# Optimization experiments

Measured on AMD Instinct MI355X. Metric: run time of the kernel, lower is better.

## Reference

```python
import jax, jax.numpy as jnp
import numpy as np
from functools import partial

BANK = 256
ADDR = 64
OUT_C, IN_C, KH, KW = 64, 64, 3, 3
BS, H, W = 32, 128, 128


def setup_inputs() -> dict:
    key = jax.random.key(0)
    ks = jax.random.split(key, 6)
    x = jax.random.normal(ks[0], (BS, IN_C, H, W), dtype=jnp.float32)
    w_addr = jax.random.normal(ks[1], (BS, ADDR), dtype=jnp.float32)
    b_addr = jax.random.normal(ks[2], (BS, OUT_C, ADDR), dtype=jnp.float32)
    # learned parameters
    w_bank = jax.random.normal(ks[3], (BANK, OUT_C, IN_C, KH, KW), dtype=jnp.float32) * (1.0 / np.sqrt(IN_C * KH * KW))
    bound = 1.0 / np.sqrt(IN_C * KH * KW)
    b_bank = jax.random.uniform(ks[4], (BANK,), minval=-bound, maxval=bound, dtype=jnp.float32)
    address_space = jax.random.normal(ks[5], (BANK, ADDR), dtype=jnp.float32)
    return {"x": x, "w_addr": w_addr, "b_addr": b_addr, "w_bank": w_bank,
            "b_bank": b_bank, "address_space": address_space, "s": 1, "p": 1}


def _hyper_conv(x, w_addr, b_addr, w_bank, b_bank, address_space, s, p):
    # soft addressing: keys @ address_space.T -> softmax -> weighted sum of bank
    sel_w = jax.nn.softmax(w_addr @ address_space.T, axis=-1)          # [bs, bank]
    w = jnp.einsum('bn,noikl->boikl', sel_w, w_bank)                   # [bs, O, I, kh, kw]
    sel_b = jax.nn.softmax(b_addr @ address_space.T, axis=-1)          # [bs, O, bank]
    b = jnp.einsum('bon,n->bo', sel_b, b_bank)                         # [bs, O]

    def conv_one(xi, wi):
        # xi: [I, H, W], wi: [O, I, kh, kw]
        return jax.lax.conv_general_dilated(
            xi[None], wi, window_strides=(s, s), padding=[(p, p), (p, p)],
            dimension_numbers=('NCHW', 'OIHW', 'NCHW'))[0]

    o = jax.vmap(conv_one)(x, w)                                       # [bs, O, H', W']
    return o + b[:, :, None, None]


def reference(x, w_addr, b_addr, w_bank, b_bank, address_space, s, p):
    return _hyper_conv(x, w_addr, b_addr, w_bank, b_bank, address_space, int(s), int(p))
```

## Files before the change

### kernel.cpp

```cpp
#include <hip/hip_runtime.h>
#include <hip/hip_bf16.h>
#include <math.h>

#define BS   32
#define IC   64
#define OC   64
#define HH   128
#define WW   128
#define BANK 256
#define ADDR 64
#define WELEM (OC*IC*9)
#define PLANE (HH*WW)

typedef short short8 __attribute__((ext_vector_type(8)));
typedef float f32x16 __attribute__((ext_vector_type(16)));

__device__ __forceinline__ short f2bf(float f) {
    unsigned u = __builtin_bit_cast(unsigned, f);
    unsigned r = (u + 0x7FFFu + ((u >> 16) & 1u)) >> 16;
    return (short)r;
}

typedef __attribute__((address_space(3))) unsigned int lds_u32;
typedef const __attribute__((address_space(1))) unsigned int g_u32;
__device__ __forceinline__ void gload16(const short* g, short* l) {
    __builtin_amdgcn_global_load_lds((g_u32*)g, (lds_u32*)l, 16, 0, 0);
}

__global__ __launch_bounds__(BANK) void k_selw(const float* __restrict__ w_addr,
                                               const float* __restrict__ aspace,
                                               float* __restrict__ sel_w) {
    int b = blockIdx.x;
    int n = threadIdx.x;
    const float* wa = w_addr + b * ADDR;
    const float* as = aspace + n * ADDR;
    float dot = 0.f;
#pragma unroll
    for (int k = 0; k < ADDR; ++k) dot = fmaf(wa[k], as[k], dot);

    __shared__ float red[BANK];
    red[n] = dot; __syncthreads();
    for (int s = BANK / 2; s > 0; s >>= 1) {
        if (n < s) red[n] = fmaxf(red[n], red[n + s]);
        __syncthreads();
    }
    float m = red[0]; __syncthreads();
    float e = expf(dot - m);
    red[n] = e; __syncthreads();
    for (int s = BANK / 2; s > 0; s >>= 1) {
        if (n < s) red[n] += red[n + s];
        __syncthreads();
    }
    sel_w[b * BANK + n] = e / red[0];
}

__global__ __launch_bounds__(BANK) void k_bias(const float* __restrict__ b_addr,
                                               const float* __restrict__ aspace,
                                               const float* __restrict__ b_bank,
                                               float* __restrict__ bias) {
    int bo = blockIdx.x;
    int n  = threadIdx.x;
    const float* ba = b_addr + (size_t)bo * ADDR;
    const float* as = aspace + n * ADDR;
    float dot = 0.f;
#pragma unroll
    for (int k = 0; k < ADDR; ++k) dot = fmaf(ba[k], as[k], dot);

    __shared__ float red[BANK];
    red[n] = dot; __syncthreads();
    for (int s = BANK / 2; s > 0; s >>= 1) {
        if (n < s) red[n] = fmaxf(red[n], red[n + s]);
        __syncthreads();
    }
    float m = red[0]; __syncthreads();
    float e = expf(dot - m);
    red[n] = e; __syncthreads();
    for (int s = BANK / 2; s > 0; s >>= 1) {
        if (n < s) red[n] += red[n + s];
        __syncthreads();
    }
    float denom = red[0]; __syncthreads();
    red[n] = e * b_bank[n]; __syncthreads();
    for (int s = BANK / 2; s > 0; s >>= 1) {
        if (n < s) red[n] += red[n + s];
        __syncthreads();
    }
    if (n == 0) bias[bo] = red[0] / denom;
}

__global__ __launch_bounds__(256) void k_wmix(const float* __restrict__ sel_w,
                                              const float* __restrict__ w_bank,
                                              __hip_bfloat16* __restrict__ wmb) {
    __shared__ float s_red[4 * 32 * 64];

    int tid = threadIdx.x;
    int jl  = tid & 63;
    int c   = tid >> 6;
    int jb  = blockIdx.x * 64 + jl;

    int n0 = __builtin_amdgcn_readfirstlane(c * 64);
    const float* selp = sel_w + n0;

    float wv[64];
#pragma unroll
    for (int n = 0; n < 64; ++n)
        wv[n] = w_bank[(size_t)(n0 + n) * WELEM + jb];

    float acc[BS];
#pragma unroll
    for (int b = 0; b < BS; ++b) acc[b] = 0.f;
#pragma unroll
    for (int b = 0; b < BS; ++b)
#pragma unroll
        for (int n = 0; n < 64; ++n)
            acc[b] = fmaf(selp[b * BANK + n], wv[n], acc[b]);

#pragma unroll
    for (int b = 0; b < BS; ++b)
        s_red[(c * 32 + b) * 64 + jl] = acc[b];
    __syncthreads();

    int B0  = (tid * 8) & 31;
    int jl2 = (tid * 8) >> 5;
    int j   = blockIdx.x * 64 + jl2;
    int o   = j / 576;
    int rem = j - o * 576;
    int i   = rem / 9;
    int tap = rem - i * 9;
    size_t base = ((size_t)tap * 8 + (i >> 3)) * 512 + (size_t)o * 8 + (i & 7);
#pragma unroll
    for (int u = 0; u < 8; ++u) {
        int b = B0 + u;
        float v = s_red[(0 * 32 + b) * 64 + jl2] + s_red[(1 * 32 + b) * 64 + jl2]
                + s_red[(2 * 32 + b) * 64 + jl2] + s_red[(3 * 32 + b) * 64 + jl2];
        short sv = f2bf(v);
        wmb[(size_t)b * (9 * 8 * 64 * 8) + base] = *reinterpret_cast<__hip_bfloat16*>(&sv);
    }
}

__global__ __launch_bounds__(512, 2) void k_conv(const float* __restrict__ x,
                                                 const short* __restrict__ wmb,
                                                 const float* __restrict__ bias,
                                                 float* __restrict__ out) {
    __shared__ short s_x[2][4 * 2 * 132 * 8];
    __shared__ short s_w[2][9 * 2 * 64 * 8];
    __shared__ float s_bias[OC];

    int orig    = blockIdx.x;
    int logical = (orig & 7) * 256 + (orig >> 3);
    int b    = logical >> 6;
    int y0   = (logical & 63) * 2;
    int tid  = threadIdx.x;
    int lane = tid & 63;
    int wv   = tid >> 6;
    int h    = lane >> 5;
    int ln   = lane & 31;
    int wr   = wv & 1;
    int oh   = (wv >> 1) & 1;
    int ph   = wv >> 2;

    if (tid < OC) s_bias[tid] = bias[b * OC + tid];
    if (tid < 32) {
        int bf   = tid >> 4;
        int kg   = (tid >> 1) & 7;
        int col  = (tid & 1) ? 129 : 0;
        *(short8*)&s_x[bf][(kg * 132 + col) * 8] = (short8){0,0,0,0,0,0,0,0};
    }

    const float* xb   = x + (size_t)b * IC * PLANE;
    const short* wmbs = wmb + (size_t)b * 36864;

    int x_goff[2], x_lds[2]; bool x_ok[2]; int x_g[2];
#pragma unroll
    for (int k = 0; k < 2; ++k) {
        int u  = k * 512 + tid;
        int ky = u >> 8;
        int g  = (u >> 7) & 1;
        int cx = u & 127;
        int gy = y0 - 1 + ky;
        x_ok[k]   = ((unsigned)gy < (unsigned)HH);
        x_g[k]    = g;
        x_goff[k] = gy * WW + cx;
        x_lds[k]  = ((ky * 2 + g) * 132 + cx + 1) * 8;
    }

    float xr[2][8];

    auto LOADX = [&](int cc) {
#pragma unroll
        for (int k = 0; k < 2; ++k) {
            if (x_ok[k]) {
                const float* p = xb + (size_t)(cc * 16 + x_g[k] * 8) * PLANE + x_goff[k];
#pragma unroll
                for (int e = 0; e < 8; ++e) xr[k][e] = p[(size_t)e * PLANE];
            } else {
#pragma unroll
                for (int e = 0; e < 8; ++e) xr[k][e] = 0.f;
            }
        }
    };
    auto STAGEW = [&](int cc, int bf) {
        for (int s = wv; s < 18; s += 8) {
            int tap = s >> 1, g = s & 1;
            const short* gsrc = wmbs + (size_t)((tap * 8 + 2 * cc + g) * 64 + lane) * 8;
            gload16(gsrc, &s_w[bf][((tap * 2 + g) * 64) * 8]);
        }
    };
    auto STOREX = [&](int bf) {
#pragma unroll
        for (int k = 0; k < 2; ++k) {
            short8 s;
#pragma unroll
            for (int e = 0; e < 8; ++e) s[e] = f2bf(xr[k][e]);
            *(short8*)&s_x[bf][x_lds[k]] = s;
        }
    };

    f32x16 acc[2];
    acc[0] = (f32x16)0.0f;
    acc[1] = (f32x16)0.0f;

    LOADX(0);
    STAGEW(0, 0);
    STOREX(0);
    __syncthreads();

#pragma unroll
    for (int cc = 0; cc < 4; ++cc) {
        int bf = cc & 1;
        if (cc < 3) {
            LOADX(cc + 1);
            STAGEW(cc + 1, bf ^ 1);
            __builtin_amdgcn_sched_barrier(0);
        }
        const short8* xb8 = (const short8*)s_x[bf];
        const short8* wb8 = (const short8*)s_w[bf];
#pragma unroll
        for (int ky = 0; ky < 3; ++ky) {
#pragma unroll
            for (int kx = 0; kx < 3; ++kx) {
                short8 a = wb8[((ky * 3 + kx) * 2 + h) * 64 + oh * 32 + ln];
#pragma unroll
                for (int nt = 0; nt < 2; ++nt) {
                    short8 bb = xb8[((wr + ky) * 2 + h) * 132 + ph * 64 + nt * 32 + ln + kx];
                    acc[nt] = __builtin_amdgcn_mfma_f32_32x32x16_bf16(a, bb, acc[nt], 0, 0, 0);
                }
            }
        }
        if (cc < 3) STOREX(bf ^ 1);
        __syncthreads();
    }

    int y = y0 + wr;
    float* ob = out + (size_t)b * OC * PLANE;
#pragma unroll
    for (int nt = 0; nt < 2; ++nt) {
#pragma unroll
        for (int r = 0; r < 16; ++r) {
            int oc = oh * 32 + (r & 3) + 8 * (r >> 2) + 4 * h;
            int px = ph * 64 + nt * 32 + ln;
            ob[((size_t)oc * HH + y) * WW + px] = acc[nt][r] + s_bias[oc];
        }
    }
}

extern "C" void kernel_launch(void* const* d_in, const int* in_sizes, int n_in,
                              void* d_out, int out_size, void* d_ws, size_t ws_size,
                              hipStream_t stream) {
    const float* x      = (const float*)d_in[0];
    const float* w_addr = (const float*)d_in[1];
    const float* b_addr = (const float*)d_in[2];
    const float* w_bank = (const float*)d_in[3];
    const float* b_bank = (const float*)d_in[4];
    const float* aspace = (const float*)d_in[5];
    float* out = (float*)d_out;

    char* ws = (char*)d_ws;
    float*          sel_w = (float*)ws;
    float*          bias  = (float*)(ws + 32768);
    __hip_bfloat16* wmb   = (__hip_bfloat16*)(ws + 40960);

    k_selw<<<BS, BANK, 0, stream>>>(w_addr, aspace, sel_w);
    k_bias<<<BS * OC, BANK, 0, stream>>>(b_addr, aspace, b_bank, bias);
    k_wmix<<<WELEM / 64, 256, 0, stream>>>(sel_w, w_bank, wmb);
    k_conv<<<BS * 64, 512, 0, stream>>>(x, (const short*)wmb, bias, out);
}
```

Baseline: 129.0 us.

## Load weights directly to registers and repack x LDS as bf16 pairs

Drops LDS staging of the weights. Each wave now reads its 9 weight fragments straight from global memory into registers every channel chunk. The x tile is reorganised in LDS as packed bf16 channel pairs, filled by vectorized float4 loads along the width, and the MFMA B operand is assembled from four scalar LDS reads. Shared memory shrinks and launch bounds go up to 4 blocks per CU for more occupancy. The cost is more global weight traffic, extra LDS read instructions per MFMA, and the loss of the unrolled outer loop and the sched_barrier overlap.

Result: slower. 135.5 us (+5.0%).

```diff
diff --git a/kernel.cpp b/kernel.cpp
--- a/kernel.cpp
+++ b/kernel.cpp
@@ -13,6 +13,7 @@
 #define PLANE (HH*WW)
 
 typedef short short8 __attribute__((ext_vector_type(8)));
+typedef int   i32x4  __attribute__((ext_vector_type(4)));
 typedef float f32x16 __attribute__((ext_vector_type(16)));
 
 __device__ __forceinline__ short f2bf(float f) {
@@ -21,10 +22,12 @@
     return (short)r;
 }
 
-typedef __attribute__((address_space(3))) unsigned int lds_u32;
-typedef const __attribute__((address_space(1))) unsigned int g_u32;
-__device__ __forceinline__ void gload16(const short* g, short* l) {
-    __builtin_amdgcn_global_load_lds((g_u32*)g, (lds_u32*)l, 16, 0, 0);
+__device__ __forceinline__ int pack_bf2(float lo, float hi) {
+    unsigned ul = __builtin_bit_cast(unsigned, lo);
+    unsigned uh = __builtin_bit_cast(unsigned, hi);
+    unsigned rl = (ul + 0x7FFFu + ((ul >> 16) & 1u)) >> 16;
+    unsigned rh = (uh + 0x7FFFu + ((uh >> 16) & 1u)) & 0xFFFF0000u;
+    return (int)(rh | (rl & 0xFFFFu));
 }
 
 __global__ __launch_bounds__(BANK) void k_selw(const float* __restrict__ w_addr,
@@ -138,12 +141,11 @@
     }
 }
 
-__global__ __launch_bounds__(512, 2) void k_conv(const float* __restrict__ x,
+__global__ __launch_bounds__(512, 4) void k_conv(const float* __restrict__ x,
                                                  const short* __restrict__ wmb,
                                                  const float* __restrict__ bias,
                                                  float* __restrict__ out) {
-    __shared__ short s_x[2][4 * 2 * 132 * 8];
-    __shared__ short s_w[2][9 * 2 * 64 * 8];
+    __shared__ int  s_x[2][4 * 2 * 4 * 136];
     __shared__ float s_bias[OC];
 
     int orig    = blockIdx.x;
@@ -160,59 +162,54 @@
     int ph   = wv >> 2;
 
     if (tid < OC) s_bias[tid] = bias[b * OC + tid];
-    if (tid < 32) {
-        int bf   = tid >> 4;
-        int kg   = (tid >> 1) & 7;
-        int col  = (tid & 1) ? 129 : 0;
-        *(short8*)&s_x[bf][(kg * 132 + col) * 8] = (short8){0,0,0,0,0,0,0,0};
+    if (tid < 128) {
+        int buf  = tid >> 6;
+        int row  = (tid & 63) >> 1;
+        int slot = (tid & 1) ? 132 : 3;
+        s_x[buf][row * 136 + slot] = 0;
     }
 
     const float* xb   = x + (size_t)b * IC * PLANE;
     const short* wmbs = wmb + (size_t)b * 36864;
 
-    int x_goff[2], x_lds[2]; bool x_ok[2]; int x_g[2];
+    int x_goff[2], x_lds[2], x_icb[2]; bool x_ok[2];
 #pragma unroll
     for (int k = 0; k < 2; ++k) {
         int u  = k * 512 + tid;
         int ky = u >> 8;
         int g  = (u >> 7) & 1;
-        int cx = u & 127;
+        int p  = (u >> 5) & 3;
+        int q  = u & 31;
         int gy = y0 - 1 + ky;
         x_ok[k]   = ((unsigned)gy < (unsigned)HH);
-        x_g[k]    = g;
-        x_goff[k] = gy * WW + cx;
-        x_lds[k]  = ((ky * 2 + g) * 132 + cx + 1) * 8;
-    }
-
-    float xr[2][8];
+        x_icb[k]  = g * 8 + 2 * p;
+        x_goff[k] = gy * WW + 4 * q;
+        x_lds[k]  = ((ky * 2 + g) * 4 + p) * 136 + 4 + 4 * q;
+    }
+
+    float4 xlo[2], xhi[2];
 
     auto LOADX = [&](int cc) {
 #pragma unroll
         for (int k = 0; k < 2; ++k) {
             if (x_ok[k]) {
-                const float* p = xb + (size_t)(cc * 16 + x_g[k] * 8) * PLANE + x_goff[k];
-#pragma unroll
-                for (int e = 0; e < 8; ++e) xr[k][e] = p[(size_t)e * PLANE];
+                const float* p = xb + (size_t)(cc * 16 + x_icb[k]) * PLANE + x_goff[k];
+                xlo[k] = *(const float4*)p;
+                xhi[k] = *(const float4*)(p + PLANE);
             } else {
-#pragma unroll
-                for (int e = 0; e < 8; ++e) xr[k][e] = 0.f;
+                xlo[k] = make_float4(0.f, 0.f, 0.f, 0.f);
+                xhi[k] = make_float4(0.f, 0.f, 0.f, 0.f);
             }
-        }
-    };
-    auto STAGEW = [&](int cc, int bf) {
-        for (int s = wv; s < 18; s += 8) {
-            int tap = s >> 1, g = s & 1;
-            const short* gsrc = wmbs + (size_t)((tap * 8 + 2 * cc + g) * 64 + lane) * 8;
-            gload16(gsrc, &s_w[bf][((tap * 2 + g) * 64) * 8]);
         }
     };
     auto STOREX = [&](int bf) {
 #pragma unroll
         for (int k = 0; k < 2; ++k) {
-            short8 s;
-#pragma unroll
-            for (int e = 0; e < 8; ++e) s[e] = f2bf(xr[k][e]);
-            *(short8*)&s_x[bf][x_lds[k]] = s;
+            i32x4 d;
+#pragma unroll
+            for (int j = 0; j < 4; ++j)
+                d[j] = pack_bf2(((const float*)&xlo[k])[j], ((const float*)&xhi[k])[j]);
+            *(i32x4*)&s_x[bf][x_lds[k]] = d;
         }
     };
 
@@ -221,28 +218,36 @@
     acc[1] = (f32x16)0.0f;
 
     LOADX(0);
-    STAGEW(0, 0);
     STOREX(0);
     __syncthreads();
 
-#pragma unroll
     for (int cc = 0; cc < 4; ++cc) {
         int bf = cc & 1;
-        if (cc < 3) {
-            LOADX(cc + 1);
-            STAGEW(cc + 1, bf ^ 1);
-            __builtin_amdgcn_sched_barrier(0);
-        }
-        const short8* xb8 = (const short8*)s_x[bf];
-        const short8* wb8 = (const short8*)s_w[bf];
+
+        short8 areg[9];
+#pragma unroll
+        for (int tap = 0; tap < 9; ++tap)
+            areg[tap] = *(const short8*)(wmbs +
+                (size_t)((tap * 8 + 2 * cc + h) * 64 + oh * 32 + ln) * 8);
+
+        if (cc < 3) LOADX(cc + 1);
+
+        const int* xi = (const int*)s_x[bf];
 #pragma unroll
         for (int ky = 0; ky < 3; ++ky) {
 #pragma unroll
             for (int kx = 0; kx < 3; ++kx) {
-                short8 a = wb8[((ky * 3 + kx) * 2 + h) * 64 + oh * 32 + ln];
+                short8 a = areg[ky * 3 + kx];
 #pragma unroll
                 for (int nt = 0; nt < 2; ++nt) {
-                    short8 bb = xb8[((wr + ky) * 2 + h) * 132 + ph * 64 + nt * 32 + ln + kx];
+                    int px   = ph * 64 + nt * 32 + ln;
+                    int base = (((wr + ky) * 2 + h) * 4) * 136 + px + kx + 3;
+                    i32x4 d;
+                    d[0] = xi[base];
+                    d[1] = xi[base + 136];
+                    d[2] = xi[base + 272];
+                    d[3] = xi[base + 408];
+                    short8 bb = __builtin_bit_cast(short8, d);
                     acc[nt] = __builtin_amdgcn_mfma_f32_32x32x16_bf16(a, bb, acc[nt], 0, 0, 0);
                 }
             }
```
